# Optimization experiments

Measured on AMD Instinct MI355X. Metric: run time of the kernel, lower is better.

The kernel has to match this reference:

```python
import jax, jax.numpy as jnp
import numpy as np

N, D, H = 4096, 1024, 16
HD = D // H  # head_dim = 64


def setup_inputs() -> dict:
    key = jax.random.key(0)
    ks = jax.random.split(key, 9)
    w_scale = 1.0 / np.sqrt(D)
    x = jax.random.normal(ks[0], (N, D), dtype=jnp.float32)
    Wq = jax.random.normal(ks[1], (D, D), dtype=jnp.float32) * w_scale
    bq = jax.random.normal(ks[2], (D,), dtype=jnp.float32) * w_scale
    Wk = jax.random.normal(ks[3], (D, D), dtype=jnp.float32) * w_scale
    bk = jax.random.normal(ks[4], (D,), dtype=jnp.float32) * w_scale
    Wv = jax.random.normal(ks[5], (D, D), dtype=jnp.float32) * w_scale
    bv = jax.random.normal(ks[6], (D,), dtype=jnp.float32) * w_scale
    Wo = jax.random.normal(ks[7], (D, D), dtype=jnp.float32) * w_scale
    bo = jax.random.normal(ks[8], (D,), dtype=jnp.float32) * w_scale
    return {"x": x, "Wq": Wq, "bq": bq, "Wk": Wk, "bk": bk,
            "Wv": Wv, "bv": bv, "Wo": Wo, "bo": bo}


def reference(x, Wq, bq, Wk, bk, Wv, bv, Wo, bo):
    # eqx.nn.Linear applies y = W @ x + b per token; vmapped over tokens -> x @ W.T + b
    q = (x @ Wq.T + bq).reshape(N, H, HD).transpose(1, 0, 2)  # [H, N, hd]
    k = (x @ Wk.T + bk).reshape(N, H, HD).transpose(1, 0, 2)  # [H, N, hd]
    v = (x @ Wv.T + bv).reshape(N, H, HD).transpose(1, 0, 2)  # [H, N, hd]
    scale = 1.0 / np.sqrt(HD)
    scores = jnp.einsum('hnd,hmd->hnm', q * scale, k)         # [H, N, N]
    attn = jax.nn.softmax(scores, axis=-1)
    ctx = jnp.einsum('hnm,hmd->hnd', attn, v)                 # [H, N, hd]
    ctx = ctx.transpose(1, 0, 2).reshape(N, D)                # [N, D]
    return ctx @ Wo.T + bo
```

## Files before the change

### kernel.cpp

```cpp
#include <hip/hip_runtime.h>
#include <hip/hip_bf16.h>

typedef __attribute__((ext_vector_type(8))) short short8;
typedef __attribute__((ext_vector_type(4))) float f32x4;
typedef __attribute__((ext_vector_type(16))) float f32x16;

#define MFMA16(a, b, c) __builtin_amdgcn_mfma_f32_16x16x32_bf16(a, b, c, 0, 0, 0)
#define MFMA32(a, b, c) __builtin_amdgcn_mfma_f32_32x32x16_bf16(a, b, c, 0, 0, 0)

typedef __attribute__((address_space(1))) const unsigned int GU32;
typedef __attribute__((address_space(3))) unsigned int LU32;
#define GLOAD16(g, l) __builtin_amdgcn_global_load_lds((GU32*)(g), (LU32*)(l), 16, 0, 0)

__device__ __forceinline__ unsigned short f2bf(float f) {
    union { float f; unsigned u; } a; a.f = f;
    unsigned r = a.u + 0x7fffu + ((a.u >> 16) & 1u);
    return (unsigned short)(r >> 16);
}

__device__ __forceinline__ unsigned pk2(float a, float b) {
    unsigned r;
    asm("v_cvt_pk_bf16_f32 %0, %1, %2" : "=v"(r) : "v"(a), "v"(b));
    return r;
}

#define CTXP_STRIDE (17u * 1024u * 1024u / 4u)

__global__ void cvt_all_k(const float* __restrict__ x,
                          const float* __restrict__ wq, const float* __restrict__ wk,
                          const float* __restrict__ wv, const float* __restrict__ wo,
                          unsigned short* __restrict__ xb,
                          unsigned short* __restrict__ wqb, unsigned short* __restrict__ wkb,
                          unsigned short* __restrict__ wvb, unsigned short* __restrict__ wob) {
    const int X4 = 4096 * 1024 / 4;
    const int W4 = 1024 * 1024 / 4;
    int i = blockIdx.x * 256 + threadIdx.x;
    const float* s; unsigned short* d; int off;
    if (i < X4) { s = x; d = xb; off = i; }
    else {
        int j = i - X4, w = j >> 18; off = j & (W4 - 1);
        s = w == 0 ? wq : (w == 1 ? wk : (w == 2 ? wv : wo));
        d = w == 0 ? wqb : (w == 1 ? wkb : (w == 2 ? wvb : wob));
    }
    float4 v = reinterpret_cast<const float4*>(s)[off];
    ushort4 o;
    o.x = f2bf(v.x); o.y = f2bf(v.y); o.z = f2bf(v.z); o.w = f2bf(v.w);
    reinterpret_cast<ushort4*>(d)[off] = o;
}

template<int MODE>
__global__ __launch_bounds__(256) void gemm_bt_k(
    const unsigned short* __restrict__ A,
    const unsigned short* __restrict__ B0, const unsigned short* __restrict__ B1,
    const unsigned short* __restrict__ B2,
    const float* __restrict__ bias0, const float* __restrict__ bias1, const float* __restrict__ bias2,
    float s0, float s1, float s2,
    void* o0, void* o1, void* o2)
{
    const int z = blockIdx.z;
    const unsigned short* B = z == 0 ? B0 : (z == 1 ? B1 : B2);
    const float* bias       = z == 0 ? bias0 : (z == 1 ? bias1 : bias2);
    const float scl         = z == 0 ? s0 : (z == 1 ? s1 : s2);
    void* outp              = z == 0 ? o0 : (z == 1 ? o1 : o2);

    __shared__ unsigned short As[2][4096];
    __shared__ unsigned short Bs[2][4096];

    const int tid = threadIdx.x;
    const int wid = tid >> 6, lane = tid & 63;
    const int lr = lane & 15, g = lane >> 4;
    const int wr = wid >> 1, wc = wid & 1;
    const int row0 = blockIdx.x * 128;
    const int col0 = blockIdx.y * 128;

    const int srow = tid >> 2;
    const int scol = (tid & 3) * 8;
    const unsigned short* aS0 = A + (row0 + srow) * 1024 + scol;
    const unsigned short* aS1 = aS0 + 64 * 1024;
    const unsigned short* bS0 = B + (col0 + srow) * 1024 + scol;
    const unsigned short* bS1 = bS0 + 64 * 1024;
    unsigned short* lA = &As[0][wid * 512];
    unsigned short* lB = &Bs[0][wid * 512];

#define GSTG(BUF, K0) do {                              \
        GLOAD16(aS0 + (K0), lA + (BUF) * 4096);         \
        GLOAD16(aS1 + (K0), lA + (BUF) * 4096 + 2048);  \
        GLOAD16(bS0 + (K0), lB + (BUF) * 4096);         \
        GLOAD16(bS1 + (K0), lB + (BUF) * 4096 + 2048);  \
    } while (0)

    f32x4 acc[4][4] = {};

    auto cmp = [&](const unsigned short* Ab, const unsigned short* Bb) {
        short8 af[4], bfr[4];
#pragma unroll
        for (int m = 0; m < 4; ++m)
            af[m] = *(const short8*)(Ab + (wr * 64 + m * 16 + lr) * 32 + g * 8);
#pragma unroll
        for (int n = 0; n < 4; ++n)
            bfr[n] = *(const short8*)(Bb + (wc * 64 + n * 16 + lr) * 32 + g * 8);
#pragma unroll
        for (int m = 0; m < 4; ++m)
#pragma unroll
            for (int n = 0; n < 4; ++n)
                acc[m][n] = MFMA16(af[m], bfr[n], acc[m][n]);
    };

    GSTG(0, 0);
    __syncthreads();
    for (int k0 = 0; k0 < 1024; k0 += 64) {
        if (k0 + 32 < 1024) GSTG(1, k0 + 32);
        cmp(As[0], Bs[0]);
        __syncthreads();
        if (k0 + 64 < 1024) GSTG(0, k0 + 64);
        cmp(As[1], Bs[1]);
        __syncthreads();
    }
#undef GSTG

    const bool vtrans = (MODE == 0) && (z == 2);
#pragma unroll
    for (int n = 0; n < 4; ++n) {
        const int col = col0 + wc * 64 + n * 16 + lr;
        const float bv = bias[col];
#pragma unroll
        for (int m = 0; m < 4; ++m) {
            if (vtrans) {
                const int base16 = row0 + wr * 64 + m * 16;
                const int gp = ((g & 1) << 1) | (g >> 1);
                float v0 = acc[m][n][0] + bv, v1 = acc[m][n][1] + bv;
                float v2 = acc[m][n][2] + bv, v3 = acc[m][n][3] + bv;
                uint2 o; o.x = pk2(v0, v1); o.y = pk2(v2, v3);
                *(uint2*)((unsigned short*)outp + col * 4096 + base16 + gp * 4) = o;
            } else {
#pragma unroll
                for (int r = 0; r < 4; ++r) {
                    const int row = row0 + wr * 64 + m * 16 + g * 4 + r;
                    const float v = (acc[m][n][r] + bv) * scl;
                    if (MODE == 1) ((float*)outp)[row * 1024 + col] = v;
                    else           ((unsigned short*)outp)[row * 1024 + col] = f2bf(v);
                }
            }
        }
    }
}

template<int SPLIT>
__global__ __launch_bounds__(256, 2) void attn_core_k(
    const unsigned short* __restrict__ Q, const unsigned short* __restrict__ K,
    const unsigned short* __restrict__ Vt, unsigned short* __restrict__ C,
    float* __restrict__ ctxp, float* __restrict__ Lb)
{
    __shared__ unsigned short Ks[2][4096];
    __shared__ unsigned short Vs[2][4096];

    int h, q0, kvz;
    if (SPLIT == 2) {
        const int lin = blockIdx.x;
        const int xcd = lin & 7, slot = lin >> 3;
        const int grp = xcd * 4 + (slot >> 4);
        h   = grp & 15;
        kvz = grp >> 4;
        q0  = (slot & 15) * 256;
    } else {
        h = blockIdx.y; kvz = 0; q0 = blockIdx.x * 256;
    }
    const int NKV = 4096 / SPLIT;
    const int kvbase = kvz * NKV;
    const int tid = threadIdx.x, w = tid >> 6, lane = tid & 63;
    const int l31 = lane & 31, hi = lane >> 5;
    const int swz = (l31 & 7) << 4;
    const int qbase = q0 + w * 64;

    const int sr = tid >> 3;
    const int sb = (tid & 7) * 16;
    const int sc = (sb ^ ((sr & 7) << 4)) >> 1;
    const unsigned short* gK0 = K  + (size_t)(kvbase + sr) * 1024 + h * 64 + sc;
    const unsigned short* gK1 = gK0 + 32 * 1024;
    const unsigned short* gV0 = Vt + (size_t)(h * 64 + sr) * 4096 + kvbase + sc;
    const unsigned short* gV1 = gV0 + 32 * 4096;
    unsigned short* kd = &Ks[0][w * 512];
    unsigned short* vd = &Vs[0][w * 512];

#define ASTAGE(BUF, KV) do {                                          \
        GLOAD16(gK0 + (size_t)(KV) * 1024, kd + (BUF) * 4096);        \
        GLOAD16(gK1 + (size_t)(KV) * 1024, kd + (BUF) * 4096 + 2048); \
        GLOAD16(gV0 + (KV),        vd + (BUF) * 4096);                \
        GLOAD16(gV1 + (KV),        vd + (BUF) * 4096 + 2048);         \
    } while (0)

    short8 qfA[4], qfB[4];
    {
        const unsigned short* qpA = Q + (size_t)(qbase + l31) * 1024 + h * 64 + hi * 8;
        const unsigned short* qpB = qpA + 32 * 1024;
#pragma unroll
        for (int c = 0; c < 4; ++c) {
            qfA[c] = *(const short8*)(qpA + c * 16);
            qfB[c] = *(const short8*)(qpB + c * 16);
        }
    }

    int koff[4];
#pragma unroll
    for (int c = 0; c < 4; ++c) koff[c] = ((c * 32 + hi * 16) ^ swz) >> 1;

    f32x16 accA0 = {}, accA1 = {}, accB0 = {}, accB1 = {};
    float lhA = 0.f, lhB = 0.f;

    auto smx = [&](f32x16& s0, f32x16& s1, float& lh, unsigned* pf) {
        float p[32];
#pragma unroll
        for (int i = 0; i < 16; ++i) {
            p[i]      = __builtin_amdgcn_exp2f(s0[i]);
            p[16 + i] = __builtin_amdgcn_exp2f(s1[i]);
        }
        float u0 = 0.f, u1 = 0.f, u2 = 0.f, u3 = 0.f;
#pragma unroll
        for (int i = 0; i < 8; ++i) {
            u0 += p[i]; u1 += p[8 + i]; u2 += p[16 + i]; u3 += p[24 + i];
        }
        lh += (u0 + u1) + (u2 + u3);
#pragma unroll
        for (int c = 0; c < 4; ++c)
#pragma unroll
            for (int u = 0; u < 4; ++u)
                pf[c * 4 + u] = pk2(p[c * 8 + u * 2], p[c * 8 + u * 2 + 1]);
    };

    auto tile = [&](const unsigned short* Kc, const unsigned short* Vc) {
        f32x16 sA0 = {}, sA1 = {}, sB0 = {}, sB1 = {};
        __builtin_amdgcn_s_setprio(1);
#pragma unroll
        for (int c = 0; c < 4; ++c) {
            const short8 k0 = *(const short8*)(Kc + l31 * 64 + koff[c]);
            const short8 k1 = *(const short8*)(Kc + 2048 + l31 * 64 + koff[c]);
            sA0 = MFMA32(k0, qfA[c], sA0);
            sA1 = MFMA32(k1, qfA[c], sA1);
            sB0 = MFMA32(k0, qfB[c], sB0);
            sB1 = MFMA32(k1, qfB[c], sB1);
        }
        __builtin_amdgcn_s_setprio(0);
        unsigned pfA[16], pfB[16];
        smx(sA0, sA1, lhA, pfA);
        smx(sB0, sB1, lhB, pfB);
        __builtin_amdgcn_s_setprio(1);
#pragma unroll
        for (int c = 0; c < 4; ++c) {
            const short8 v0 = *(const short8*)(Vc + l31 * 64 + koff[c]);
            const short8 v1 = *(const short8*)(Vc + 2048 + l31 * 64 + koff[c]);
            union { unsigned u[4]; short8 s; } pA, pB;
#pragma unroll
            for (int u = 0; u < 4; ++u) { pA.u[u] = pfA[c * 4 + u]; pB.u[u] = pfB[c * 4 + u]; }
            accA0 = MFMA32(v0, pA.s, accA0);
            accA1 = MFMA32(v1, pA.s, accA1);
            accB0 = MFMA32(v0, pB.s, accB0);
            accB1 = MFMA32(v1, pB.s, accB1);
        }
        __builtin_amdgcn_s_setprio(0);
    };

    ASTAGE(0, 0);
    __syncthreads();
    for (int kv = 0; kv < NKV; kv += 128) {
        if (kv + 64 < NKV) ASTAGE(1, kv + 64);
        tile(Ks[0], Vs[0]);
        __syncthreads();
        if (kv + 128 < NKV) ASTAGE(0, kv + 128);
        tile(Ks[1], Vs[1]);
        __syncthreads();
    }
#undef ASTAGE

    const float lA = lhA + __shfl_xor(lhA, 32);
    const float lB = lhB + __shfl_xor(lhB, 32);

    if (SPLIT == 1) {
        const float liA = 1.f / lA, liB = 1.f / lB;
        unsigned short* CpA = C + (size_t)(qbase + l31) * 1024 + h * 64;
        unsigned short* CpB = CpA + 32 * 1024;
#pragma unroll
        for (int dt = 0; dt < 2; ++dt)
#pragma unroll
            for (int rq = 0; rq < 4; ++rq) {
                const f32x16& aA = dt ? accA1 : accA0;
                const f32x16& aB = dt ? accB1 : accB0;
                uint2 oA, oB;
                oA.x = pk2(aA[rq * 4 + 0] * liA, aA[rq * 4 + 1] * liA);
                oA.y = pk2(aA[rq * 4 + 2] * liA, aA[rq * 4 + 3] * liA);
                oB.x = pk2(aB[rq * 4 + 0] * liB, aB[rq * 4 + 1] * liB);
                oB.y = pk2(aB[rq * 4 + 2] * liB, aB[rq * 4 + 3] * liB);
                *(uint2*)(CpA + dt * 32 + rq * 8 + hi * 4) = oA;
                *(uint2*)(CpB + dt * 32 + rq * 8 + hi * 4) = oB;
            }
    } else {
        float* OpA = ctxp + (size_t)kvz * CTXP_STRIDE + (size_t)(qbase + l31) * 1024 + h * 64;
        float* OpB = OpA + 32 * 1024;
#pragma unroll
        for (int dt = 0; dt < 2; ++dt)
#pragma unroll
            for (int rq = 0; rq < 4; ++rq) {
                const f32x16& aA = dt ? accA1 : accA0;
                const f32x16& aB = dt ? accB1 : accB0;
                *(float4*)(OpA + dt * 32 + rq * 8 + hi * 4) =
                    make_float4(aA[rq * 4 + 0], aA[rq * 4 + 1], aA[rq * 4 + 2], aA[rq * 4 + 3]);
                *(float4*)(OpB + dt * 32 + rq * 8 + hi * 4) =
                    make_float4(aB[rq * 4 + 0], aB[rq * 4 + 1], aB[rq * 4 + 2], aB[rq * 4 + 3]);
            }
        const int q = qbase + hi * 32 + l31;
        Lb[((size_t)kvz * 16 + h) * 4096 + q] = hi ? lB : lA;
    }
}

template<int NS>
__global__ __launch_bounds__(256) void combine_k(
    const float* __restrict__ ctxp, const float* __restrict__ Lb,
    unsigned short* __restrict__ C)
{
    int idx = blockIdx.x * 256 + threadIdx.x;
    int q = idx >> 7, d0 = (idx & 127) * 8, h = d0 >> 6;
    float L = 0.f;
#pragma unroll
    for (int z = 0; z < NS; ++z) L += Lb[((size_t)z * 16 + h) * 4096 + q];
    const float inv = 1.f / L;
    float4 s0 = make_float4(0.f, 0.f, 0.f, 0.f), s1 = s0;
#pragma unroll
    for (int z = 0; z < NS; ++z) {
        const float4* p = (const float4*)(ctxp + (size_t)z * CTXP_STRIDE + (size_t)q * 1024 + d0);
        float4 a = p[0], b = p[1];
        s0.x += a.x; s0.y += a.y; s0.z += a.z; s0.w += a.w;
        s1.x += b.x; s1.y += b.y; s1.z += b.z; s1.w += b.w;
    }
    uint4 o;
    o.x = pk2(s0.x * inv, s0.y * inv);
    o.y = pk2(s0.z * inv, s0.w * inv);
    o.z = pk2(s1.x * inv, s1.y * inv);
    o.w = pk2(s1.z * inv, s1.w * inv);
    *(uint4*)(C + (size_t)q * 1024 + d0) = o;
}

extern "C" void kernel_launch(void* const* d_in, const int* in_sizes, int n_in,
                              void* d_out, int out_size, void* d_ws, size_t ws_size,
                              hipStream_t stream) {
    const float* x  = (const float*)d_in[0];
    const float* Wq = (const float*)d_in[1];
    const float* bq = (const float*)d_in[2];
    const float* Wk = (const float*)d_in[3];
    const float* bk = (const float*)d_in[4];
    const float* Wv = (const float*)d_in[5];
    const float* bv = (const float*)d_in[6];
    const float* Wo = (const float*)d_in[7];
    const float* bo = (const float*)d_in[8];
    float* out = (float*)d_out;

    const size_t MB = 1ull << 20;
    char* ws = (char*)d_ws;
    unsigned short* xb  = (unsigned short*)(ws);
    unsigned short* Wqb = (unsigned short*)(ws + 8 * MB);
    unsigned short* Wkb = (unsigned short*)(ws + 10 * MB);
    unsigned short* Wvb = (unsigned short*)(ws + 12 * MB);
    unsigned short* Wob = (unsigned short*)(ws + 14 * MB);
    unsigned short* Qb  = (unsigned short*)(ws + 16 * MB);
    unsigned short* Kb  = (unsigned short*)(ws + 24 * MB);
    unsigned short* Vtb = (unsigned short*)(ws + 32 * MB);
    unsigned short* Cb  = xb;
    float* ctxp = (float*)(ws + 40 * MB);
    float* Lb2  = (float*)(ws + 74 * MB);

    cvt_all_k<<<8192, 256, 0, stream>>>(x, Wq, Wk, Wv, Wo, xb, Wqb, Wkb, Wvb, Wob);

    const float qscale = 0.125f * 1.4426950408889634f;
    gemm_bt_k<0><<<dim3(32, 8, 3), 256, 0, stream>>>(xb, Wqb, Wkb, Wvb, bq, bk, bv,
                                                     qscale, 1.f, 1.f, Qb, Kb, Vtb);

    if (ws_size >= 76 * MB) {
        attn_core_k<2><<<dim3(512, 1, 1), 256, 0, stream>>>(Qb, Kb, Vtb, Cb, ctxp, Lb2);
        combine_k<2><<<2048, 256, 0, stream>>>(ctxp, Lb2, Cb);
    } else {
        attn_core_k<1><<<dim3(16, 16, 1), 256, 0, stream>>>(Qb, Kb, Vtb, Cb, nullptr, nullptr);
    }

    gemm_bt_k<1><<<dim3(32, 8, 1), 256, 0, stream>>>(Cb, Wob, Wob, Wob, bo, bo, bo,
                                                     1.f, 1.f, 1.f, out, out, out);
}
```

Before: 148.9 us.

## Fuse split-KV combine and normalization into output projection GEMM A-load

Replaces the separate combine kernel and the bf16 context buffer with a new output GEMM. It loads both fp32 partial contexts and their softmax denominators, sums and normalizes them, converts to bf16 and writes straight into LDS. This removes one launch and the round trip of the bf16 context through global memory. In exchange, each column block re-reads the fp32 partials (recomputing the reciprocal of the denominators), which multiplies global/L2 traffic for the A operand and uses register-staged rather than async loads.

```diff
diff --git a/kernel.cpp b/kernel.cpp
--- a/kernel.cpp
+++ b/kernel.cpp
@@ -145,6 +145,123 @@
     }
 }
 
+__global__ __launch_bounds__(256) void gemm_out_fused_k(
+    const float* __restrict__ ctxp, const float* __restrict__ Lb,
+    const unsigned short* __restrict__ B, const float* __restrict__ bias,
+    float* __restrict__ outp)
+{
+    __shared__ unsigned short As[2][4096];
+    __shared__ unsigned short Bs[2][4096];
+
+    const int tid = threadIdx.x;
+    const int wid = tid >> 6, lane = tid & 63;
+    const int lr = lane & 15, g = lane >> 4;
+    const int wr = wid >> 1, wc = wid & 1;
+    const int row0 = blockIdx.x * 128;
+    const int col0 = blockIdx.y * 128;
+
+    const int srow = tid >> 2;
+    const int scol = (tid & 3) * 8;
+    const int r0 = row0 + srow, r1 = r0 + 64;
+    const unsigned short* bS0 = B + (col0 + srow) * 1024 + scol;
+    const unsigned short* bS1 = bS0 + 64 * 1024;
+    unsigned short* lB = &Bs[0][wid * 512];
+    unsigned short* wA = &As[0][wid * 512 + (lane & 63) * 8];
+
+    struct AStage { float4 p0, p1, q0, q1, u0, u1, v0, v1; float il0, il1; };
+
+    auto loadA = [&](AStage& st, int k0) {
+        const int col = k0 + scol;
+        const int hh = col >> 6;
+        const float* L0 = Lb + (size_t)hh * 4096;
+        const float* L1 = Lb + (size_t)(16 + hh) * 4096;
+        st.il0 = 1.f / (L0[r0] + L1[r0]);
+        st.il1 = 1.f / (L0[r1] + L1[r1]);
+        const float* a0 = ctxp + (size_t)r0 * 1024 + col;
+        const float* a1 = ctxp + CTXP_STRIDE + (size_t)r0 * 1024 + col;
+        const float* b0 = ctxp + (size_t)r1 * 1024 + col;
+        const float* b1 = ctxp + CTXP_STRIDE + (size_t)r1 * 1024 + col;
+        st.p0 = *(const float4*)a0;  st.p1 = *(const float4*)(a0 + 4);
+        st.q0 = *(const float4*)a1;  st.q1 = *(const float4*)(a1 + 4);
+        st.u0 = *(const float4*)b0;  st.u1 = *(const float4*)(b0 + 4);
+        st.v0 = *(const float4*)b1;  st.v1 = *(const float4*)(b1 + 4);
+    };
+    auto writeA = [&](int buf, const AStage& st) {
+        uint4 o0, o1;
+        o0.x = pk2((st.p0.x + st.q0.x) * st.il0, (st.p0.y + st.q0.y) * st.il0);
+        o0.y = pk2((st.p0.z + st.q0.z) * st.il0, (st.p0.w + st.q0.w) * st.il0);
+        o0.z = pk2((st.p1.x + st.q1.x) * st.il0, (st.p1.y + st.q1.y) * st.il0);
+        o0.w = pk2((st.p1.z + st.q1.z) * st.il0, (st.p1.w + st.q1.w) * st.il0);
+        o1.x = pk2((st.u0.x + st.v0.x) * st.il1, (st.u0.y + st.v0.y) * st.il1);
+        o1.y = pk2((st.u0.z + st.v0.z) * st.il1, (st.u0.w + st.v0.w) * st.il1);
+        o1.z = pk2((st.u1.x + st.v1.x) * st.il1, (st.u1.y + st.v1.y) * st.il1);
+        o1.w = pk2((st.u1.z + st.v1.z) * st.il1, (st.u1.w + st.v1.w) * st.il1);
+        *(uint4*)(wA + buf * 4096)        = o0;
+        *(uint4*)(wA + buf * 4096 + 2048) = o1;
+    };
+
+    f32x4 acc[4][4] = {};
+
+    auto cmp = [&](const unsigned short* Ab, const unsigned short* Bb) {
+        short8 af[4], bfr[4];
+#pragma unroll
+        for (int m = 0; m < 4; ++m)
+            af[m] = *(const short8*)(Ab + (wr * 64 + m * 16 + lr) * 32 + g * 8);
+#pragma unroll
+        for (int n = 0; n < 4; ++n)
+            bfr[n] = *(const short8*)(Bb + (wc * 64 + n * 16 + lr) * 32 + g * 8);
+#pragma unroll
+        for (int m = 0; m < 4; ++m)
+#pragma unroll
+            for (int n = 0; n < 4; ++n)
+                acc[m][n] = MFMA16(af[m], bfr[n], acc[m][n]);
+    };
+
+    {
+        AStage st;
+        loadA(st, 0);
+        GLOAD16(bS0, lB);
+        GLOAD16(bS1, lB + 2048);
+        writeA(0, st);
+    }
+    __syncthreads();
+    for (int k0 = 0; k0 < 1024; k0 += 64) {
+        {
+            AStage st;
+            loadA(st, k0 + 32);
+            GLOAD16(bS0 + k0 + 32, lB + 4096);
+            GLOAD16(bS1 + k0 + 32, lB + 4096 + 2048);
+            cmp(As[0], Bs[0]);
+            writeA(1, st);
+        }
+        __syncthreads();
+        if (k0 + 64 < 1024) {
+            AStage st;
+            loadA(st, k0 + 64);
+            GLOAD16(bS0 + k0 + 64, lB);
+            GLOAD16(bS1 + k0 + 64, lB + 2048);
+            cmp(As[1], Bs[1]);
+            writeA(0, st);
+        } else {
+            cmp(As[1], Bs[1]);
+        }
+        __syncthreads();
+    }
+
+#pragma unroll
+    for (int n = 0; n < 4; ++n) {
+        const int col = col0 + wc * 64 + n * 16 + lr;
+        const float bv = bias[col];
+#pragma unroll
+        for (int m = 0; m < 4; ++m)
+#pragma unroll
+            for (int r = 0; r < 4; ++r) {
+                const int row = row0 + wr * 64 + m * 16 + g * 4 + r;
+                outp[(size_t)row * 1024 + col] = acc[m][n][r] + bv;
+            }
+    }
+}
+
 template<int SPLIT>
 __global__ __launch_bounds__(256, 2) void attn_core_k(
     const unsigned short* __restrict__ Q, const unsigned short* __restrict__ K,
@@ -311,30 +428,22 @@
     }
 }
 
-template<int NS>
 __global__ __launch_bounds__(256) void combine_k(
     const float* __restrict__ ctxp, const float* __restrict__ Lb,
     unsigned short* __restrict__ C)
 {
     int idx = blockIdx.x * 256 + threadIdx.x;
     int q = idx >> 7, d0 = (idx & 127) * 8, h = d0 >> 6;
-    float L = 0.f;
-#pragma unroll
-    for (int z = 0; z < NS; ++z) L += Lb[((size_t)z * 16 + h) * 4096 + q];
+    float L = Lb[(size_t)h * 4096 + q] + Lb[(size_t)(16 + h) * 4096 + q];
     const float inv = 1.f / L;
-    float4 s0 = make_float4(0.f, 0.f, 0.f, 0.f), s1 = s0;
-#pragma unroll
-    for (int z = 0; z < NS; ++z) {
-        const float4* p = (const float4*)(ctxp + (size_t)z * CTXP_STRIDE + (size_t)q * 1024 + d0);
-        float4 a = p[0], b = p[1];
-        s0.x += a.x; s0.y += a.y; s0.z += a.z; s0.w += a.w;
-        s1.x += b.x; s1.y += b.y; s1.z += b.z; s1.w += b.w;
-    }
+    const float4* p0 = (const float4*)(ctxp + (size_t)q * 1024 + d0);
+    const float4* p1 = (const float4*)(ctxp + CTXP_STRIDE + (size_t)q * 1024 + d0);
+    float4 a0 = p0[0], a1 = p0[1], b0 = p1[0], b1 = p1[1];
     uint4 o;
-    o.x = pk2(s0.x * inv, s0.y * inv);
-    o.y = pk2(s0.z * inv, s0.w * inv);
-    o.z = pk2(s1.x * inv, s1.y * inv);
-    o.w = pk2(s1.z * inv, s1.w * inv);
+    o.x = pk2((a0.x + b0.x) * inv, (a0.y + b0.y) * inv);
+    o.y = pk2((a0.z + b0.z) * inv, (a0.w + b0.w) * inv);
+    o.z = pk2((a1.x + b1.x) * inv, (a1.y + b1.y) * inv);
+    o.w = pk2((a1.z + b1.z) * inv, (a1.w + b1.w) * inv);
     *(uint4*)(C + (size_t)q * 1024 + d0) = o;
 }
 
@@ -374,11 +483,10 @@
 
     if (ws_size >= 76 * MB) {
         attn_core_k<2><<<dim3(512, 1, 1), 256, 0, stream>>>(Qb, Kb, Vtb, Cb, ctxp, Lb2);
-        combine_k<2><<<2048, 256, 0, stream>>>(ctxp, Lb2, Cb);
+        gemm_out_fused_k<<<dim3(32, 8), 256, 0, stream>>>(ctxp, Lb2, Wob, bo, out);
     } else {
         attn_core_k<1><<<dim3(16, 16, 1), 256, 0, stream>>>(Qb, Kb, Vtb, Cb, nullptr, nullptr);
-    }
-
-    gemm_bt_k<1><<<dim3(32, 8, 1), 256, 0, stream>>>(Cb, Wob, Wob, Wob, bo, bo, bo,
-                                                     1.f, 1.f, 1.f, out, out, out);
-}
+        gemm_bt_k<1><<<dim3(32, 8, 1), 256, 0, stream>>>(Cb, Wob, Wob, Wob, bo, bo, bo,
+                                                         1.f, 1.f, 1.f, out, out, out);
+    }
+}
```

After: 157.4 us. 1.06x slower.
